# Kernel tuning notes

Hardware: AMD Instinct MI355X
Metric: run time of the kernel (lower is better)

The kernel has to match this reference:

```python
import jax, jax.numpy as jnp
import numpy as np
from jax import lax

WINDOW_SIZE = 11
SIGMA = 1.5
MAX_VAL = 1.0
C1 = (MAX_VAL * 0.01) ** 2
C2 = (MAX_VAL * 0.03) ** 2


def _make_window(channel: int, k: int = WINDOW_SIZE, sigma: float = SIGMA) -> np.ndarray:
    x = np.arange(k, dtype=np.float64)
    g = np.exp(-((x - k // 2) ** 2) / (2.0 * sigma ** 2))
    g = (g / g.sum()).astype(np.float32)
    # rank-1 separable 3D window, built as dense [C,1,k,k,k] kernel (OIDHW, groups=C)
    w3 = g[:, None, None] * g[None, :, None] * g[None, None, :]
    return np.broadcast_to(w3, (channel, 1, k, k, k)).copy()


def _dwconv3d(x, kernel, pad):
    # depthwise 3D conv, SAME padding for odd kernel
    return lax.conv_general_dilated(
        x, kernel, window_strides=(1, 1, 1), padding=[(pad, pad)] * 3,
        dimension_numbers=("NCDHW", "OIDHW", "NCDHW"),
        feature_group_count=kernel.shape[0])


def setup_inputs() -> dict:
    key = jax.random.key(0)
    k1, k2 = jax.random.split(key)
    shape = (2, 4, 64, 160, 160)  # [B, C, D, H, W]
    img1 = jax.random.uniform(k1, shape, dtype=jnp.float32)
    img2 = jax.random.uniform(k2, shape, dtype=jnp.float32)
    return {"img1": img1, "img2": img2}


def reference(img1, img2):
    channel = img1.shape[1]
    window = jnp.asarray(_make_window(channel))
    pad = WINDOW_SIZE // 2
    # mask = ones_like(img1) in the original -> identity multiply, omitted
    mu1 = _dwconv3d(img1, window, pad)
    mu2 = _dwconv3d(img2, window, pad)
    mu1_sq = mu1 * mu1
    mu2_sq = mu2 * mu2
    mu1_mu2 = mu1 * mu2
    sigma1_sq = _dwconv3d(img1 * img1, window, pad) - mu1_sq
    sigma2_sq = _dwconv3d(img2 * img2, window, pad) - mu2_sq
    sigma12 = _dwconv3d(img1 * img2, window, pad) - mu1_mu2
    ssim_map = ((2.0 * mu1_mu2 + C1) * (2.0 * sigma12 + C2)) / (
        (mu1_sq + mu2_sq + C1) * (sigma1_sq + sigma2_sq + C2))
    ssim = jnp.mean(ssim_map, axis=(0, 2, 3, 4))  # per-channel SSIM, shape [C]
    return 1.0 - ssim
```

## Files before the change

### kernel.cpp

```cpp
#include <hip/hip_runtime.h>
#include <math.h>

typedef float v2f __attribute__((ext_vector_type(2)));

namespace {

constexpr int C_DIM = 4;
constexpr int D_DIM = 64;
constexpr int H_DIM = 160;
constexpr int W_DIM = 160;

constexpr int TH = 20;
constexpr int TW = 20;
constexpr int HALO = 5;
constexpr int EH = 30;
constexpr int EW = 30;
constexpr int XST = 31;
constexpr int MST = 21;
constexpr int NPIX = EH * EW;

constexpr int TILES_W = 8;
constexpr int TPC = 64;
constexpr int NBLOCKS = 2 * C_DIM * TPC;

constexpr float C1f = 1e-4f;
constexpr float C2f = 9e-4f;
constexpr float INV_N = 1.0f / (2.0f * 64.0f * 160.0f * 160.0f);

struct GW { float g[11]; };

}

__global__ void finalize_kernel(const float* __restrict__ partial,
                                float* __restrict__ out) {
    const int tid = threadIdx.x;
    const int c = tid >> 6;
    const int lane = tid & 63;
    float s = partial[c * TPC + lane] +
              partial[C_DIM * TPC + c * TPC + lane];
#pragma unroll
    for (int off = 32; off > 0; off >>= 1) s += __shfl_down(s, off, 64);
    if (lane == 0 && c < C_DIM) out[c] = 1.0f - s * INV_N;
}

__global__ __launch_bounds__(256, 2) void ssim3d_kernel(
    const float* __restrict__ img1, const float* __restrict__ img2,
    float* __restrict__ partial, GW gwp) {

    const int bid = blockIdx.x;
    const int tile = bid % TPC;
    const int c = (bid / TPC) % C_DIM;
    const int b = bid / (TPC * C_DIM);
    const int h0 = (tile / TILES_W) * TH;
    const int w0 = (tile % TILES_W) * TW;

    const long planeHW = (long)H_DIM * W_DIM;
    const long volbase = (long)(b * C_DIM + c) * D_DIM * planeHW;
    const long org = volbase + (long)(h0 - HALO) * W_DIM + (w0 - HALO);
    const float* __restrict__ p1 = img1 + org;
    const float* __restrict__ p2 = img2 + org;

    const bool interior = (h0 >= HALO) && (h0 + TH + HALO <= H_DIM) &&
                          (w0 >= HALO) && (w0 + TW + HALO <= W_DIM);

    __shared__ v2f    xy[2][EH][XST];
    __shared__ float4 mid[2][EH][MST];
    __shared__ float  rbuf[4];

    const int tid = threadIdx.x;

    int hh_[4], ww_[4], off_[4];
    bool live_[4], ok_[4];
#pragma unroll
    for (int k = 0; k < 4; ++k) {
        const int e = tid + k * 256;
        live_[k] = (e < NPIX);
        const int hh = e / EW;
        const int ww = e - hh * EW;
        hh_[k] = hh; ww_[k] = ww;
        off_[k] = hh * W_DIM + ww;
        const int gh = h0 - HALO + hh;
        const int gw = w0 - HALO + ww;
        ok_[k] = ((unsigned)gh < (unsigned)H_DIM) &&
                 ((unsigned)gw < (unsigned)W_DIM);
    }

    auto fetch_slice = [&](int s, v2f lv[4]) {
        const long sb = (long)s * planeHW;
#pragma unroll
        for (int k = 0; k < 4; ++k) {
            lv[k] = (v2f){0.0f, 0.0f};
            if (live_[k] && (interior || ok_[k])) {
                const long gi = sb + off_[k];
                lv[k].x = p1[gi];
                lv[k].y = p2[gi];
            }
        }
    };
    auto commit_slice = [&](int buf, const v2f lv[4]) {
#pragma unroll
        for (int k = 0; k < 4; ++k)
            if (live_[k]) xy[buf][hh_[k]][ww_[k]] = lv[k];
    };

    const bool wactive = (tid < 150);
    const int whh = tid % 30;
    const int wg  = (tid / 30) * 4;

    auto wconv = [&](int cur) {
        v2f a0 = {0.f,0.f}, a1 = {0.f,0.f}, a2 = {0.f,0.f}, a3 = {0.f,0.f};
        v2f q0 = {0.f,0.f}, q1 = {0.f,0.f}, q2 = {0.f,0.f}, q3 = {0.f,0.f};
#pragma unroll
        for (int t = 0; t < 14; ++t) {
            const v2f xv = xy[cur][whh][wg + t];
            v2f qp;
            qp.x = fmaf(xv.x, xv.x, xv.y * xv.y);
            qp.y = xv.x * xv.y;
            if (t <= 10) {
                const v2f g2 = {gwp.g[t], gwp.g[t]};
                a0 = __builtin_elementwise_fma(g2, xv, a0);
                q0 = __builtin_elementwise_fma(g2, qp, q0);
            }
            if (t >= 1 && t <= 11) {
                const v2f g2 = {gwp.g[t-1], gwp.g[t-1]};
                a1 = __builtin_elementwise_fma(g2, xv, a1);
                q1 = __builtin_elementwise_fma(g2, qp, q1);
            }
            if (t >= 2 && t <= 12) {
                const v2f g2 = {gwp.g[t-2], gwp.g[t-2]};
                a2 = __builtin_elementwise_fma(g2, xv, a2);
                q2 = __builtin_elementwise_fma(g2, qp, q2);
            }
            if (t >= 3) {
                const v2f g2 = {gwp.g[t-3], gwp.g[t-3]};
                a3 = __builtin_elementwise_fma(g2, xv, a3);
                q3 = __builtin_elementwise_fma(g2, qp, q3);
            }
        }
        mid[cur][whh][wg]     = make_float4(a0.x, a0.y, q0.x, q0.y);
        mid[cur][whh][wg + 1] = make_float4(a1.x, a1.y, q1.x, q1.y);
        mid[cur][whh][wg + 2] = make_float4(a2.x, a2.y, q2.x, q2.y);
        mid[cur][whh][wg + 3] = make_float4(a3.x, a3.y, q3.x, q3.y);
    };

    const bool hworker = (tid < 200);
    const int hw = tid % 20;
    const int hb = (tid / 20) * 2;

    float accum = 0.0f;
    auto ssim_add = [&](v2f mxy, v2f mqp) {
        const float m1 = mxy.x, m2 = mxy.y;
        const float q = mqp.x, pp = mqp.y;
        const float m1s = m1 * m1;
        const float m2s = m2 * m2;
        const float m12 = m1 * m2;
        const float spp = q - m1s - m2s;
        const float s12 = pp - m12;
        const float num = (2.0f * m12 + C1f) * (2.0f * s12 + C2f);
        const float den = (m1s + m2s + C1f) * (spp + C2f);
        accum = fmaf(num, __builtin_amdgcn_rcpf(den), accum);
    };

    v2f w0xy[14], w0qp[14], w1xy[14], w1qp[14];
#pragma unroll
    for (int i = 0; i < 14; ++i) {
        w0xy[i] = (v2f){0.f, 0.f}; w0qp[i] = (v2f){0.f, 0.f};
        w1xy[i] = (v2f){0.f, 0.f}; w1qp[i] = (v2f){0.f, 0.f};
    }

    {
        v2f lv[4];
        fetch_slice(0, lv);
        commit_slice(0, lv);
    }
    __syncthreads();

    for (int sb = 0; sb < D_DIM; sb += 4) {
#pragma unroll
        for (int u = 0; u < 4; ++u) {
            const int s = sb + u;
            v2f lv[4];
            const bool have_next = (s + 1 < D_DIM);
            if (have_next) fetch_slice(s + 1, lv);
            if (wactive) wconv(u & 1);
            if (have_next) commit_slice((u + 1) & 1, lv);
            __syncthreads();
            if (hworker) {
                v2f z0x = {0.f,0.f}, z0q = {0.f,0.f};
                v2f z1x = {0.f,0.f}, z1q = {0.f,0.f};
#pragma unroll
                for (int t = 0; t < 12; ++t) {
                    const float4 m = mid[u & 1][hb + t][hw];
                    const v2f ma = {m.x, m.y};
                    const v2f mb = {m.z, m.w};
                    if (t <= 10) {
                        const v2f g2 = {gwp.g[t], gwp.g[t]};
                        z0x = __builtin_elementwise_fma(g2, ma, z0x);
                        z0q = __builtin_elementwise_fma(g2, mb, z0q);
                    }
                    if (t >= 1) {
                        const v2f g2 = {gwp.g[t-1], gwp.g[t-1]};
                        z1x = __builtin_elementwise_fma(g2, ma, z1x);
                        z1q = __builtin_elementwise_fma(g2, mb, z1q);
                    }
                }
                w0xy[10 + u] = z0x; w0qp[10 + u] = z0q;
                w1xy[10 + u] = z1x; w1qp[10 + u] = z1q;
                if (s >= HALO) {
                    v2f mx0 = {0.f,0.f}, mq0 = {0.f,0.f};
                    v2f mx1 = {0.f,0.f}, mq1 = {0.f,0.f};
#pragma unroll
                    for (int t = 0; t < 11; ++t) {
                        const v2f g2 = {gwp.g[t], gwp.g[t]};
                        mx0 = __builtin_elementwise_fma(g2, w0xy[u + t], mx0);
                        mq0 = __builtin_elementwise_fma(g2, w0qp[u + t], mq0);
                        mx1 = __builtin_elementwise_fma(g2, w1xy[u + t], mx1);
                        mq1 = __builtin_elementwise_fma(g2, w1qp[u + t], mq1);
                    }
                    ssim_add(mx0, mq0);
                    ssim_add(mx1, mq1);
                }
            }
        }
        if (hworker) {
#pragma unroll
            for (int k = 0; k < 10; ++k) {
                w0xy[k] = w0xy[k + 4]; w0qp[k] = w0qp[k + 4];
                w1xy[k] = w1xy[k + 4]; w1qp[k] = w1qp[k + 4];
            }
        }
    }

    if (hworker) {
#pragma unroll
        for (int i = 10; i < 14; ++i) {
            w0xy[i] = (v2f){0.f, 0.f}; w0qp[i] = (v2f){0.f, 0.f};
            w1xy[i] = (v2f){0.f, 0.f}; w1qp[i] = (v2f){0.f, 0.f};
        }
#pragma unroll
        for (int u2 = 0; u2 < 5; ++u2) {
            v2f mx0 = {0.f,0.f}, mq0 = {0.f,0.f};
            v2f mx1 = {0.f,0.f}, mq1 = {0.f,0.f};
#pragma unroll
            for (int t = 0; t < 11; ++t) {
                if (u2 + t <= 13) {
                    const v2f g2 = {gwp.g[t], gwp.g[t]};
                    mx0 = __builtin_elementwise_fma(g2, w0xy[u2 + t], mx0);
                    mq0 = __builtin_elementwise_fma(g2, w0qp[u2 + t], mq0);
                    mx1 = __builtin_elementwise_fma(g2, w1xy[u2 + t], mx1);
                    mq1 = __builtin_elementwise_fma(g2, w1qp[u2 + t], mq1);
                }
            }
            ssim_add(mx0, mq0);
            ssim_add(mx1, mq1);
        }
    }

#pragma unroll
    for (int off = 32; off > 0; off >>= 1) accum += __shfl_down(accum, off, 64);
    const int wave = tid >> 6;
    const int lane = tid & 63;
    if (lane == 0) rbuf[wave] = accum;
    __syncthreads();
    if (tid == 0) partial[bid] = rbuf[0] + rbuf[1] + rbuf[2] + rbuf[3];
}

extern "C" void kernel_launch(void* const* d_in, const int* in_sizes, int n_in,
                              void* d_out, int out_size, void* d_ws, size_t ws_size,
                              hipStream_t stream) {
    const float* img1 = (const float*)d_in[0];
    const float* img2 = (const float*)d_in[1];
    float* out = (float*)d_out;
    float* partial = (float*)d_ws;

    GW gw;
    {
        double gd[11];
        double ssum = 0.0;
        for (int i = 0; i < 11; ++i) {
            const double t = (double)(i - 5);
            gd[i] = exp(-(t * t) / 4.5);
            ssum += gd[i];
        }
        for (int i = 0; i < 11; ++i) gw.g[i] = (float)(gd[i] / ssum);
    }

    ssim3d_kernel<<<NBLOCKS, 256, 0, stream>>>(img1, img2, partial, gw);
    finalize_kernel<<<1, 256, 0, stream>>>(partial, out);
}
```

Measured before the change: 208.0 us.

## Split depth axis across blocks with halo recompute to raise parallelism

Each tile's depth range is split into two halves processed by separate blocks, with a 5-slice halo recomputed on each side. The depth loop becomes a unified phase function that handles out-of-range slices as zeros, and the finalize kernel sums the extra partials. Launch bounds are raised to four blocks per CU. The aim is more blocks and better occupancy on a GPU with many CUs, at the cost of redundant halo work and tighter register limits.

```diff
diff --git a/kernel.cpp b/kernel.cpp
--- a/kernel.cpp
+++ b/kernel.cpp
@@ -21,7 +21,10 @@
 
 constexpr int TILES_W = 8;
 constexpr int TPC = 64;
-constexpr int NBLOCKS = 2 * C_DIM * TPC;
+constexpr int DSPLIT = 2;
+constexpr int DLEN = D_DIM / DSPLIT;
+constexpr int NPHASE = DLEN + 2 * HALO;
+constexpr int NBLOCKS = 2 * C_DIM * DSPLIT * TPC;
 
 constexpr float C1f = 1e-4f;
 constexpr float C2f = 9e-4f;
@@ -36,23 +39,30 @@
     const int tid = threadIdx.x;
     const int c = tid >> 6;
     const int lane = tid & 63;
-    float s = partial[c * TPC + lane] +
-              partial[C_DIM * TPC + c * TPC + lane];
+    float s = 0.0f;
+#pragma unroll
+    for (int b = 0; b < 2; ++b)
+#pragma unroll
+        for (int dh = 0; dh < DSPLIT; ++dh)
+            s += partial[(((b * C_DIM + c) * DSPLIT) + dh) * TPC + lane];
 #pragma unroll
     for (int off = 32; off > 0; off >>= 1) s += __shfl_down(s, off, 64);
     if (lane == 0 && c < C_DIM) out[c] = 1.0f - s * INV_N;
 }
 
-__global__ __launch_bounds__(256, 2) void ssim3d_kernel(
+__global__ __launch_bounds__(256, 4) void ssim3d_kernel(
     const float* __restrict__ img1, const float* __restrict__ img2,
     float* __restrict__ partial, GW gwp) {
 
     const int bid = blockIdx.x;
     const int tile = bid % TPC;
-    const int c = (bid / TPC) % C_DIM;
-    const int b = bid / (TPC * C_DIM);
+    const int rest = bid / TPC;
+    const int dh = rest % DSPLIT;
+    const int c = (rest / DSPLIT) % C_DIM;
+    const int b = rest / (DSPLIT * C_DIM);
     const int h0 = (tile / TILES_W) * TH;
     const int w0 = (tile % TILES_W) * TW;
+    const int d0 = dh * DLEN;
 
     const long planeHW = (long)H_DIM * W_DIM;
     const long volbase = (long)(b * C_DIM + c) * D_DIM * planeHW;
@@ -85,8 +95,8 @@
                  ((unsigned)gw < (unsigned)W_DIM);
     }
 
-    auto fetch_slice = [&](int s, v2f lv[4]) {
-        const long sb = (long)s * planeHW;
+    auto fetch_slice = [&](int gs, v2f lv[4]) {
+        const long sb = (long)gs * planeHW;
 #pragma unroll
         for (int k = 0; k < 4; ++k) {
             lv[k] = (v2f){0.0f, 0.0f};
@@ -168,26 +178,20 @@
         w1xy[i] = (v2f){0.f, 0.f}; w1qp[i] = (v2f){0.f, 0.f};
     }
 
-    {
+    auto phase = [&](int ls, int u) {
+        const int gs = d0 - HALO + ls;
+        const bool active = (gs >= 0) && (gs < D_DIM);
+        const int gsn = gs + 1;
+        const bool nactive = (ls + 1 < NPHASE) && (gsn >= 0) && (gsn < D_DIM);
         v2f lv[4];
-        fetch_slice(0, lv);
-        commit_slice(0, lv);
-    }
-    __syncthreads();
-
-    for (int sb = 0; sb < D_DIM; sb += 4) {
-#pragma unroll
-        for (int u = 0; u < 4; ++u) {
-            const int s = sb + u;
-            v2f lv[4];
-            const bool have_next = (s + 1 < D_DIM);
-            if (have_next) fetch_slice(s + 1, lv);
-            if (wactive) wconv(u & 1);
-            if (have_next) commit_slice((u + 1) & 1, lv);
-            __syncthreads();
-            if (hworker) {
-                v2f z0x = {0.f,0.f}, z0q = {0.f,0.f};
-                v2f z1x = {0.f,0.f}, z1q = {0.f,0.f};
+        if (nactive) fetch_slice(gsn, lv);
+        if (active && wactive) wconv(u & 1);
+        if (nactive) commit_slice((u + 1) & 1, lv);
+        __syncthreads();
+        if (hworker) {
+            v2f z0x = {0.f,0.f}, z0q = {0.f,0.f};
+            v2f z1x = {0.f,0.f}, z1q = {0.f,0.f};
+            if (active) {
 #pragma unroll
                 for (int t = 0; t < 12; ++t) {
                     const float4 m = mid[u & 1][hb + t][hw];
@@ -204,24 +208,39 @@
                         z1q = __builtin_elementwise_fma(g2, mb, z1q);
                     }
                 }
-                w0xy[10 + u] = z0x; w0qp[10 + u] = z0q;
-                w1xy[10 + u] = z1x; w1qp[10 + u] = z1q;
-                if (s >= HALO) {
-                    v2f mx0 = {0.f,0.f}, mq0 = {0.f,0.f};
-                    v2f mx1 = {0.f,0.f}, mq1 = {0.f,0.f};
-#pragma unroll
-                    for (int t = 0; t < 11; ++t) {
-                        const v2f g2 = {gwp.g[t], gwp.g[t]};
-                        mx0 = __builtin_elementwise_fma(g2, w0xy[u + t], mx0);
-                        mq0 = __builtin_elementwise_fma(g2, w0qp[u + t], mq0);
-                        mx1 = __builtin_elementwise_fma(g2, w1xy[u + t], mx1);
-                        mq1 = __builtin_elementwise_fma(g2, w1qp[u + t], mq1);
-                    }
-                    ssim_add(mx0, mq0);
-                    ssim_add(mx1, mq1);
+            }
+            w0xy[10 + u] = z0x; w0qp[10 + u] = z0q;
+            w1xy[10 + u] = z1x; w1qp[10 + u] = z1q;
+            if (ls >= 10) {
+                v2f mx0 = {0.f,0.f}, mq0 = {0.f,0.f};
+                v2f mx1 = {0.f,0.f}, mq1 = {0.f,0.f};
+#pragma unroll
+                for (int t = 0; t < 11; ++t) {
+                    const v2f g2 = {gwp.g[t], gwp.g[t]};
+                    mx0 = __builtin_elementwise_fma(g2, w0xy[u + t], mx0);
+                    mq0 = __builtin_elementwise_fma(g2, w0qp[u + t], mq0);
+                    mx1 = __builtin_elementwise_fma(g2, w1xy[u + t], mx1);
+                    mq1 = __builtin_elementwise_fma(g2, w1qp[u + t], mq1);
                 }
-            }
-        }
+                ssim_add(mx0, mq0);
+                ssim_add(mx1, mq1);
+            }
+        }
+    };
+
+    {
+        const int gs0 = d0 - HALO;
+        if (gs0 >= 0) {
+            v2f lv[4];
+            fetch_slice(gs0, lv);
+            commit_slice(0, lv);
+        }
+    }
+    __syncthreads();
+
+    for (int sb = 0; sb < 40; sb += 4) {
+#pragma unroll
+        for (int u = 0; u < 4; ++u) phase(sb + u, u);
         if (hworker) {
 #pragma unroll
             for (int k = 0; k < 10; ++k) {
@@ -230,31 +249,8 @@
             }
         }
     }
-
-    if (hworker) {
-#pragma unroll
-        for (int i = 10; i < 14; ++i) {
-            w0xy[i] = (v2f){0.f, 0.f}; w0qp[i] = (v2f){0.f, 0.f};
-            w1xy[i] = (v2f){0.f, 0.f}; w1qp[i] = (v2f){0.f, 0.f};
-        }
-#pragma unroll
-        for (int u2 = 0; u2 < 5; ++u2) {
-            v2f mx0 = {0.f,0.f}, mq0 = {0.f,0.f};
-            v2f mx1 = {0.f,0.f}, mq1 = {0.f,0.f};
-#pragma unroll
-            for (int t = 0; t < 11; ++t) {
-                if (u2 + t <= 13) {
-                    const v2f g2 = {gwp.g[t], gwp.g[t]};
-                    mx0 = __builtin_elementwise_fma(g2, w0xy[u2 + t], mx0);
-                    mq0 = __builtin_elementwise_fma(g2, w0qp[u2 + t], mq0);
-                    mx1 = __builtin_elementwise_fma(g2, w1xy[u2 + t], mx1);
-                    mq1 = __builtin_elementwise_fma(g2, w1qp[u2 + t], mq1);
-                }
-            }
-            ssim_add(mx0, mq0);
-            ssim_add(mx1, mq1);
-        }
-    }
+#pragma unroll
+    for (int u = 0; u < 2; ++u) phase(40 + u, u);
 
 #pragma unroll
     for (int off = 32; off > 0; off >>= 1) accum += __shfl_down(accum, off, 64);
```

After: 557.9 us. 168% more time.
